# Kernel tuning notes

Measured on AMD Instinct MI355X. Metric: run time of the kernel, lower is better.

## Reference

```python
import jax, jax.numpy as jnp
import numpy as np
import math

D, H, B, T = 1024, 16, 2, 2048
DH = D // H


def setup_inputs() -> dict:
    key = jax.random.key(0)
    ks = jax.random.split(key, 9)
    s = 1.0 / math.sqrt(D)
    x = jax.random.normal(ks[0], (B, T, D), dtype=jnp.float32)
    # True = masked position (masked_fill semantics); causal mask broadcast over b, h
    mask = jnp.triu(jnp.ones((T, T), dtype=bool), k=1)[None, None, :, :]
    wq = jax.random.normal(ks[1], (D, D), dtype=jnp.float32) * s
    bq = jnp.zeros((D,), dtype=jnp.float32)
    wk = jax.random.normal(ks[2], (D, D), dtype=jnp.float32) * s
    bk = jnp.zeros((D,), dtype=jnp.float32)
    wv = jax.random.normal(ks[3], (D, D), dtype=jnp.float32) * s
    bv = jnp.zeros((D,), dtype=jnp.float32)
    wo = jax.random.normal(ks[4], (D, D), dtype=jnp.float32) * s
    bo = jnp.zeros((D,), dtype=jnp.float32)
    return {"x": x, "mask": mask, "wq": wq, "bq": bq, "wk": wk, "bk": bk,
            "wv": wv, "bv": bv, "wo": wo, "bo": bo}


def _rotate_half(u):
    h = u.shape[-1] // 2
    return jnp.concatenate([-u[..., h:], u[..., :h]], axis=-1)


def _sincos(t, dh, dtype):
    pos = jnp.arange(t, dtype=dtype)[:, None]                    # [t, 1]
    inv = 1.0 / (10000.0 ** (jnp.arange(0, dh, 2, dtype=dtype) / dh))  # [dh/2]
    ang = pos * inv                                              # [t, dh/2]
    sin = jnp.repeat(jnp.sin(ang), 2, axis=-1)                   # [t, dh]
    cos = jnp.repeat(jnp.cos(ang), 2, axis=-1)
    return sin, cos


def reference(x, mask, wq, bq, wk, bk, wv, bv, wo, bo):
    b, t, d = x.shape
    h, dh = H, DH
    def heads(u):  # [b,t,d] -> [b,h,t,dh]
        return u.reshape(b, t, h, dh).transpose(0, 2, 1, 3)
    q = heads(x @ wq + bq)
    k = heads(x @ wk + bk)
    v = heads(x @ wv + bv)
    sin, cos = _sincos(t, dh, x.dtype)                           # [t, dh]
    q = q * cos + _rotate_half(q) * sin
    k = k * cos + _rotate_half(k) * sin
    a = jnp.einsum('bhqd,bhkd->bhqk', q, k) / jnp.sqrt(jnp.asarray(dh, x.dtype))
    a = jnp.where(mask, jnp.asarray(-10000.0, x.dtype), a)
    a = jax.nn.softmax(a, axis=-1)                               # dropout p=0.0 -> identity
    out = jnp.einsum('bhqk,bhkd->bhqd', a, v)
    out = out.transpose(0, 2, 1, 3).reshape(b, t, d)
    return out @ wo + bo
```

## Files before the change

### kernel.cpp

```cpp
#include <hip/hip_runtime.h>
#include <hip/hip_bf16.h>

#define DD 1024
#define HH 16
#define BB 2
#define TT 2048
#define DHH 64
#define MM (BB * TT)
#define NQT (TT / 64)
#define BKG 32

typedef __attribute__((ext_vector_type(8))) short bfrag;
typedef __attribute__((ext_vector_type(4))) float ffrag;

__device__ __forceinline__ unsigned short f2bf(float f) {
    __hip_bfloat16 h = __float2bfloat16(f);
    return *reinterpret_cast<unsigned short*>(&h);
}

__device__ __forceinline__ void gl_lds16(const unsigned short* g, unsigned short* l) {
    __builtin_amdgcn_global_load_lds(
        (const __attribute__((address_space(1))) unsigned int*)g,
        (__attribute__((address_space(3))) unsigned int*)l, 16, 0, 0);
}

__global__ __launch_bounds__(256) void prepass_kernel(
    const float* __restrict__ x, unsigned short* __restrict__ xb,
    const float* __restrict__ wq, const float* __restrict__ wk,
    const float* __restrict__ wv, const float* __restrict__ wo,
    unsigned short* __restrict__ oq, unsigned short* __restrict__ ok,
    unsigned short* __restrict__ ov, unsigned short* __restrict__ oo,
    float2* __restrict__ rope_tab)
{
    __shared__ float T[64][65];
    const int z = blockIdx.z;
    const int t = threadIdx.x;
    if (z == 4) {
        const int bid = blockIdx.y * 16 + blockIdx.x;
#pragma unroll
        for (int g = 0; g < 16; ++g) {
            int i = bid * 4096 + g * 256 + t;
            float4 v = ((const float4*)x)[i];
            ushort4 o;
            o.x = f2bf(v.x); o.y = f2bf(v.y); o.z = f2bf(v.z); o.w = f2bf(v.w);
            ((ushort4*)xb)[i] = o;
        }
        int idx = bid * 256 + t;
        int tpos = idx >> 5, i = idx & 31;
        float inv = __expf(-(float)i * (9.210340371976184f / 32.0f));
        float ang = (float)tpos * inv;
        float sv, cv;
        sincosf(ang, &sv, &cv);
        rope_tab[idx] = make_float2(cv, sv);
        return;
    }
    const float* W    = (z == 0) ? wq : (z == 1) ? wk : (z == 2) ? wv : wo;
    unsigned short* O = (z == 0) ? oq : (z == 1) ? ok : (z == 2) ? ov : oo;
    const int n0 = blockIdx.x * 64, k0 = blockIdx.y * 64;
#pragma unroll
    for (int g = 0; g < 16; ++g) {
        int idx = g * 256 + t;
        int r = idx >> 6, c = idx & 63;
        T[c][r] = W[(size_t)(k0 + r) * DD + n0 + c];
    }
    __syncthreads();
#pragma unroll
    for (int g = 0; g < 16; ++g) {
        int idx = g * 256 + t;
        int r = idx >> 6, c = idx & 63;
        O[(size_t)(n0 + r) * DD + k0 + c] = f2bf(T[r][c]);
    }
}

__device__ __forceinline__ void gemm128(
    const unsigned short* __restrict__ X, const unsigned short* __restrict__ Wt,
    int m0, int n0, unsigned short* As, unsigned short* Bs, ffrag acc[4][4])
{
    const int t  = threadIdx.x;
    const int l  = t & 63, w = t >> 6;
    const int lm = l & 15, lq = l >> 4;
    const int wr = w >> 1, wc = w & 1;
    const int srow = l >> 2;
    const int scol = (l & 3) * 8;
#pragma unroll
    for (int m = 0; m < 4; ++m)
#pragma unroll
        for (int n = 0; n < 4; ++n) acc[m][n] = (ffrag){0.f, 0.f, 0.f, 0.f};

    for (int k0 = 0; k0 < DD; k0 += BKG) {
#pragma unroll
        for (int it = 0; it < 2; ++it) {
            const int row = (w * 2 + it) * 16 + srow;
            gl_lds16(&X [(size_t)(m0 + row) * DD + k0 + scol], &As[(w * 2 + it) * 512]);
            gl_lds16(&Wt[(size_t)(n0 + row) * DD + k0 + scol], &Bs[(w * 2 + it) * 512]);
        }
        __syncthreads();
        bfrag a[4], b[4];
#pragma unroll
        for (int m = 0; m < 4; ++m)
            a[m] = *(const bfrag*)&As[(wr * 64 + m * 16 + lm) * BKG + lq * 8];
#pragma unroll
        for (int n = 0; n < 4; ++n)
            b[n] = *(const bfrag*)&Bs[(wc * 64 + n * 16 + lm) * BKG + lq * 8];
#pragma unroll
        for (int m = 0; m < 4; ++m)
#pragma unroll
            for (int n = 0; n < 4; ++n)
                acc[m][n] = __builtin_amdgcn_mfma_f32_16x16x32_bf16(a[m], b[n], acc[m][n], 0, 0, 0);
        __syncthreads();
    }
}

__global__ __launch_bounds__(256) void qkv_rope_kernel(
    const unsigned short* __restrict__ xb,
    const unsigned short* __restrict__ wt_qkv,
    const float* __restrict__ bq, const float* __restrict__ bk,
    const float* __restrict__ bv, const float2* __restrict__ rope_tab,
    unsigned short* __restrict__ Qh, unsigned short* __restrict__ Kh,
    unsigned short* __restrict__ Vh)
{
    __shared__ __align__(16) unsigned short As[128 * BKG];
    __shared__ __align__(16) unsigned short Bs[128 * BKG];
    const int n0 = blockIdx.x * 128, m0 = blockIdx.y * 128;
    ffrag acc[4][4];
    gemm128(xb, wt_qkv, m0, n0, As, Bs, acc);

    const int t  = threadIdx.x;
    const int l  = t & 63, w = t >> 6;
    const int lm = l & 15, lq = l >> 4;
    const int wr = w >> 1, wc = w & 1;
    const int ncol0 = n0 + wc * 64;
    const int which = ncol0 >> 10;
    const float* bias   = (which == 0) ? bq : (which == 1) ? bk : bv;
    unsigned short* Out = (which == 0) ? Qh : (which == 1) ? Kh : Vh;
    const int h = (ncol0 & 1023) >> 6;

    float bv4[4];
#pragma unroll
    for (int n = 0; n < 4; ++n) bv4[n] = bias[(ncol0 & 1023) + n * 16 + lm];

#pragma unroll
    for (int m = 0; m < 4; ++m) {
#pragma unroll
        for (int r = 0; r < 4; ++r) {
            const int row  = m0 + wr * 64 + m * 16 + lq * 4 + r;
            const int b    = row >> 11;
            const int tpos = row & 2047;
            const int bh   = b * HH + h;
#pragma unroll
            for (int n = 0; n < 4; ++n) {
                const int j = n * 16 + lm;
                float val = acc[m][n][r] + bv4[n];
                if (which < 2) {
                    float pair = acc[m][n ^ 2][r] + bv4[n ^ 2];
                    float rh   = (j < 32) ? -pair : pair;
                    float2 cs  = rope_tab[tpos * 32 + (j >> 1)];
                    Out[((size_t)bh * TT + tpos) * DHH + j] = f2bf(val * cs.x + rh * cs.y);
                } else {
                    Out[((size_t)bh * DHH + j) * TT + tpos] = f2bf(val);
                }
            }
        }
    }
}

__global__ __launch_bounds__(256) void attn_kernel(
    const unsigned short* __restrict__ Qh, const unsigned short* __restrict__ Kh,
    const unsigned short* __restrict__ Vh, unsigned short* __restrict__ attn_out)
{
    __shared__ __align__(16) unsigned short Ks[2][64][72];
    __shared__ __align__(16) unsigned short Vt[2][64][72];
    __shared__ __align__(16) unsigned short Pl[4][16][72];

    const int bh = blockIdx.y;
    const int t  = threadIdx.x;
    const int l  = t & 63, w = t >> 6;
    const int lm = l & 15, lq = l >> 4;
    const int r0 = t >> 3, c0 = (t & 7) * 8;
    const float SCALE = 0.125f * 1.4426950408889634f;

    const unsigned short* Qb = Qh + (size_t)bh * TT * DHH;
    const unsigned short* Kb = Kh + (size_t)bh * TT * DHH;
    const unsigned short* Vb = Vh + (size_t)bh * DHH * TT;

    const bfrag onesf = (bfrag){0x3F80, 0x3F80, 0x3F80, 0x3F80,
                                0x3F80, 0x3F80, 0x3F80, 0x3F80};
    const int b = bh >> 4, h = bh & 15;

#pragma unroll 1
    for (int pi = 0; pi < 2; ++pi) {
        const int qt  = (pi == 0) ? (NQT - 1 - blockIdx.x) : blockIdx.x;
        const int q0  = qt * 64, wm0 = q0 + w * 16;

        bfrag qf[2];
#pragma unroll
        for (int kc = 0; kc < 2; ++kc)
            qf[kc] = *(const bfrag*)&Qb[(size_t)(wm0 + lm) * DHH + kc * 32 + lq * 8];

        ffrag o[4];
#pragma unroll
        for (int s = 0; s < 4; ++s) o[s] = (ffrag){0.f, 0.f, 0.f, 0.f};
        ffrag lacc = (ffrag){0.f, 0.f, 0.f, 0.f};

        uint4 pk0, pk1, pv0, pv1;
        pk0 = *(const uint4*)&Kb[(size_t)(r0) * DHH + c0];
        pk1 = *(const uint4*)&Kb[(size_t)(r0 + 32) * DHH + c0];
        pv0 = *(const uint4*)&Vb[(size_t)r0 * TT + c0];
        pv1 = *(const uint4*)&Vb[(size_t)(r0 + 32) * TT + c0];
        *(uint4*)&Ks[0][r0][c0]      = pk0;
        *(uint4*)&Ks[0][r0 + 32][c0] = pk1;
        *(uint4*)&Vt[0][r0][c0]      = pv0;
        *(uint4*)&Vt[0][r0 + 32][c0] = pv1;
        __syncthreads();

        const int nkt = qt + 1;
        for (int kt = 0; kt < nkt; ++kt) {
            const int cur = kt & 1;
            const bool pf = (kt + 1 < nkt);
            if (pf) {
                const int k1 = (kt + 1) * 64;
                pk0 = *(const uint4*)&Kb[(size_t)(k1 + r0) * DHH + c0];
                pk1 = *(const uint4*)&Kb[(size_t)(k1 + r0 + 32) * DHH + c0];
                pv0 = *(const uint4*)&Vb[(size_t)r0 * TT + k1 + c0];
                pv1 = *(const uint4*)&Vb[(size_t)(r0 + 32) * TT + k1 + c0];
            }
            const int k0 = kt * 64;

            float sv[4][4];
#pragma unroll
            for (int s = 0; s < 4; ++s) {
                ffrag sa = (ffrag){0.f, 0.f, 0.f, 0.f};
#pragma unroll
                for (int kc = 0; kc < 2; ++kc) {
                    bfrag bb = *(const bfrag*)&Ks[cur][s * 16 + lm][kc * 32 + lq * 8];
                    sa = __builtin_amdgcn_mfma_f32_16x16x32_bf16(qf[kc], bb, sa, 0, 0, 0);
                }
#pragma unroll
                for (int r = 0; r < 4; ++r)
                    sv[s][r] = sa[r] * SCALE;
            }
            if (kt == qt) {
#pragma unroll
                for (int s = 0; s < 4; ++s) {
                    const int col = k0 + s * 16 + lm;
#pragma unroll
                    for (int r = 0; r < 4; ++r) {
                        const int rowg = wm0 + lq * 4 + r;
                        if (col > rowg) sv[s][r] = -1e30f;
                    }
                }
            }
#pragma unroll
            for (int s = 0; s < 4; ++s)
#pragma unroll
                for (int r = 0; r < 4; ++r)
                    sv[s][r] = exp2f(sv[s][r]);
#pragma unroll
            for (int s = 0; s < 4; ++s) {
                const int ssw = (s ^ ((4 - lq) & 3)) * 16 + lm;
#pragma unroll
                for (int r = 0; r < 4; ++r)
                    Pl[w][lq * 4 + r][ssw] = f2bf(sv[s][r]);
            }
            asm volatile("s_waitcnt lgkmcnt(0)" ::: "memory");
            const int gsw = (4 - (lm >> 2)) & 3;
#pragma unroll
            for (int kc = 0; kc < 2; ++kc) {
                const int scol = ((kc * 2 + (lq >> 1)) ^ gsw) * 16 + (lq & 1) * 8;
                bfrag a = *(const bfrag*)&Pl[w][lm][scol];
#pragma unroll
                for (int s = 0; s < 4; ++s) {
                    bfrag bb = *(const bfrag*)&Vt[cur][s * 16 + lm][kc * 32 + lq * 8];
                    o[s] = __builtin_amdgcn_mfma_f32_16x16x32_bf16(a, bb, o[s], 0, 0, 0);
                }
                lacc = __builtin_amdgcn_mfma_f32_16x16x32_bf16(a, onesf, lacc, 0, 0, 0);
            }
            if (pf) {
                *(uint4*)&Ks[cur ^ 1][r0][c0]      = pk0;
                *(uint4*)&Ks[cur ^ 1][r0 + 32][c0] = pk1;
                *(uint4*)&Vt[cur ^ 1][r0][c0]      = pv0;
                *(uint4*)&Vt[cur ^ 1][r0 + 32][c0] = pv1;
            }
            __syncthreads();
        }

#pragma unroll
        for (int r = 0; r < 4; ++r) {
            const int trow = wm0 + lq * 4 + r;
            const float linv = 1.0f / lacc[r];
#pragma unroll
            for (int s = 0; s < 4; ++s) {
                float ov = o[s][r] * linv;
                attn_out[(((size_t)b * TT + trow) * HH + h) * DHH + s * 16 + lm] = f2bf(ov);
            }
        }
    }
}

__global__ __launch_bounds__(256) void oproj_kernel(
    const unsigned short* __restrict__ attn, const unsigned short* __restrict__ wto,
    const float* __restrict__ bo, float* __restrict__ out)
{
    __shared__ __align__(16) unsigned short As[128 * BKG];
    __shared__ __align__(16) unsigned short Bs[128 * BKG];
    const int n0 = blockIdx.x * 128, m0 = blockIdx.y * 128;
    ffrag acc[4][4];
    gemm128(attn, wto, m0, n0, As, Bs, acc);

    const int t  = threadIdx.x;
    const int l  = t & 63, w = t >> 6;
    const int lm = l & 15, lq = l >> 4;
    const int wr = w >> 1, wc = w & 1;
#pragma unroll
    for (int n = 0; n < 4; ++n) {
        const int col = n0 + wc * 64 + n * 16 + lm;
        const float bb = bo[col];
#pragma unroll
        for (int m = 0; m < 4; ++m)
#pragma unroll
            for (int r = 0; r < 4; ++r) {
                const int row = m0 + wr * 64 + m * 16 + lq * 4 + r;
                out[(size_t)row * DD + col] = acc[m][n][r] + bb;
            }
    }
}

extern "C" void kernel_launch(void* const* d_in, const int* in_sizes, int n_in,
                              void* d_out, int out_size, void* d_ws, size_t ws_size,
                              hipStream_t stream) {
    const float* x  = (const float*)d_in[0];
    const float* wq = (const float*)d_in[2];
    const float* bq = (const float*)d_in[3];
    const float* wk = (const float*)d_in[4];
    const float* bk = (const float*)d_in[5];
    const float* wv = (const float*)d_in[6];
    const float* bv = (const float*)d_in[7];
    const float* wo = (const float*)d_in[8];
    const float* bo = (const float*)d_in[9];

    const size_t perT = (size_t)BB * HH * TT * DHH;
    const size_t perW = (size_t)DD * DD;
    unsigned short* xb   = (unsigned short*)d_ws;
    unsigned short* wtq  = xb  + perT;
    unsigned short* wtk  = wtq + perW;
    unsigned short* wtv  = wtk + perW;
    unsigned short* wto  = wtv + perW;
    unsigned short* Qh   = wto + perW;
    unsigned short* Kh   = Qh + perT;
    unsigned short* Vh   = Kh + perT;
    unsigned short* attn = Vh + perT;
    float2* rope_tab     = (float2*)(attn + perT);

    prepass_kernel<<<dim3(16, 16, 5), 256, 0, stream>>>(
        x, xb, wq, wk, wv, wo, wtq, wtk, wtv, wto, rope_tab);
    qkv_rope_kernel<<<dim3(24, 32), 256, 0, stream>>>(
        xb, wtq, bq, bk, bv, rope_tab, Qh, Kh, Vh);
    attn_kernel<<<dim3(NQT / 2, 32), 256, 0, stream>>>(Qh, Kh, Vh, attn);
    oproj_kernel<<<dim3(8, 32), 256, 0, stream>>>(attn, wto, bo, (float*)d_out);
}
```

Before: 227.2 us.

## Software-pipeline PV matmul one tile behind QK with double-buffered P

```diff
diff --git a/kernel.cpp b/kernel.cpp
--- a/kernel.cpp
+++ b/kernel.cpp
@@ -170,7 +170,7 @@
 {
     __shared__ __align__(16) unsigned short Ks[2][64][72];
     __shared__ __align__(16) unsigned short Vt[2][64][72];
-    __shared__ __align__(16) unsigned short Pl[4][16][72];
+    __shared__ __align__(16) unsigned short Pl[2][4][16][72];
 
     const int bh = blockIdx.y;
     const int t  = threadIdx.x;
@@ -186,6 +186,7 @@
     const bfrag onesf = (bfrag){0x3F80, 0x3F80, 0x3F80, 0x3F80,
                                 0x3F80, 0x3F80, 0x3F80, 0x3F80};
     const int b = bh >> 4, h = bh & 15;
+    const int gsw = (4 - (lm >> 2)) & 3;
 
 #pragma unroll 1
     for (int pi = 0; pi < 2; ++pi) {
@@ -202,29 +203,27 @@
         for (int s = 0; s < 4; ++s) o[s] = (ffrag){0.f, 0.f, 0.f, 0.f};
         ffrag lacc = (ffrag){0.f, 0.f, 0.f, 0.f};
 
-        uint4 pk0, pk1, pv0, pv1;
-        pk0 = *(const uint4*)&Kb[(size_t)(r0) * DHH + c0];
-        pk1 = *(const uint4*)&Kb[(size_t)(r0 + 32) * DHH + c0];
-        pv0 = *(const uint4*)&Vb[(size_t)r0 * TT + c0];
-        pv1 = *(const uint4*)&Vb[(size_t)(r0 + 32) * TT + c0];
-        *(uint4*)&Ks[0][r0][c0]      = pk0;
-        *(uint4*)&Ks[0][r0 + 32][c0] = pk1;
-        *(uint4*)&Vt[0][r0][c0]      = pv0;
-        *(uint4*)&Vt[0][r0 + 32][c0] = pv1;
+        {
+            uint4 a0 = *(const uint4*)&Kb[(size_t)(r0) * DHH + c0];
+            uint4 a1 = *(const uint4*)&Kb[(size_t)(r0 + 32) * DHH + c0];
+            *(uint4*)&Ks[0][r0][c0]      = a0;
+            *(uint4*)&Ks[0][r0 + 32][c0] = a1;
+        }
         __syncthreads();
 
         const int nkt = qt + 1;
+#pragma unroll 1
         for (int kt = 0; kt < nkt; ++kt) {
             const int cur = kt & 1;
-            const bool pf = (kt + 1 < nkt);
-            if (pf) {
-                const int k1 = (kt + 1) * 64;
-                pk0 = *(const uint4*)&Kb[(size_t)(k1 + r0) * DHH + c0];
-                pk1 = *(const uint4*)&Kb[(size_t)(k1 + r0 + 32) * DHH + c0];
-                pv0 = *(const uint4*)&Vb[(size_t)r0 * TT + k1 + c0];
-                pv1 = *(const uint4*)&Vb[(size_t)(r0 + 32) * TT + k1 + c0];
-            }
-            const int k0 = kt * 64;
+            const int k0  = kt * 64;
+            uint4 nk0, nk1, nv0, nv1;
+            const bool pfk = (kt < qt);
+            if (pfk) {
+                nk0 = *(const uint4*)&Kb[(size_t)(k0 + 64 + r0) * DHH + c0];
+                nk1 = *(const uint4*)&Kb[(size_t)(k0 + 64 + r0 + 32) * DHH + c0];
+            }
+            nv0 = *(const uint4*)&Vb[(size_t)r0 * TT + k0 + c0];
+            nv1 = *(const uint4*)&Vb[(size_t)(r0 + 32) * TT + k0 + c0];
 
             float sv[4][4];
 #pragma unroll
@@ -255,34 +254,54 @@
 #pragma unroll
                 for (int r = 0; r < 4; ++r)
                     sv[s][r] = exp2f(sv[s][r]);
+
+            if (kt > 0) {
+                const int prv = cur ^ 1;
+#pragma unroll
+                for (int kc = 0; kc < 2; ++kc) {
+                    const int scol = ((kc * 2 + (lq >> 1)) ^ gsw) * 16 + (lq & 1) * 8;
+                    bfrag a = *(const bfrag*)&Pl[prv][w][lm][scol];
+#pragma unroll
+                    for (int s = 0; s < 4; ++s) {
+                        bfrag bb = *(const bfrag*)&Vt[prv][s * 16 + lm][kc * 32 + lq * 8];
+                        o[s] = __builtin_amdgcn_mfma_f32_16x16x32_bf16(a, bb, o[s], 0, 0, 0);
+                    }
+                    lacc = __builtin_amdgcn_mfma_f32_16x16x32_bf16(a, onesf, lacc, 0, 0, 0);
+                }
+            }
+
 #pragma unroll
             for (int s = 0; s < 4; ++s) {
                 const int ssw = (s ^ ((4 - lq) & 3)) * 16 + lm;
 #pragma unroll
                 for (int r = 0; r < 4; ++r)
-                    Pl[w][lq * 4 + r][ssw] = f2bf(sv[s][r]);
-            }
-            asm volatile("s_waitcnt lgkmcnt(0)" ::: "memory");
-            const int gsw = (4 - (lm >> 2)) & 3;
+                    Pl[cur][w][lq * 4 + r][ssw] = f2bf(sv[s][r]);
+            }
+
+            if (pfk) {
+                *(uint4*)&Ks[cur ^ 1][r0][c0]      = nk0;
+                *(uint4*)&Ks[cur ^ 1][r0 + 32][c0] = nk1;
+            }
+            *(uint4*)&Vt[cur][r0][c0]      = nv0;
+            *(uint4*)&Vt[cur][r0 + 32][c0] = nv1;
+            __syncthreads();
+        }
+
+        {
+            const int prv = qt & 1;
 #pragma unroll
             for (int kc = 0; kc < 2; ++kc) {
                 const int scol = ((kc * 2 + (lq >> 1)) ^ gsw) * 16 + (lq & 1) * 8;
-                bfrag a = *(const bfrag*)&Pl[w][lm][scol];
+                bfrag a = *(const bfrag*)&Pl[prv][w][lm][scol];
 #pragma unroll
                 for (int s = 0; s < 4; ++s) {
-                    bfrag bb = *(const bfrag*)&Vt[cur][s * 16 + lm][kc * 32 + lq * 8];
+                    bfrag bb = *(const bfrag*)&Vt[prv][s * 16 + lm][kc * 32 + lq * 8];
                     o[s] = __builtin_amdgcn_mfma_f32_16x16x32_bf16(a, bb, o[s], 0, 0, 0);
                 }
                 lacc = __builtin_amdgcn_mfma_f32_16x16x32_bf16(a, onesf, lacc, 0, 0, 0);
             }
-            if (pf) {
-                *(uint4*)&Ks[cur ^ 1][r0][c0]      = pk0;
-                *(uint4*)&Ks[cur ^ 1][r0 + 32][c0] = pk1;
-                *(uint4*)&Vt[cur ^ 1][r0][c0]      = pv0;
-                *(uint4*)&Vt[cur ^ 1][r0 + 32][c0] = pv1;
-            }
-            __syncthreads();
-        }
+        }
+        __syncthreads();
 
 #pragma unroll
         for (int r = 0; r < 4; ++r) {
```

New measurement: 227.7 us. No clear change (+0.2%).

## Keep P in registers via shuffles, fold softmax scale into Q RoPE

Applied to the files above, without the earlier changes.

```diff
diff --git a/kernel.cpp b/kernel.cpp
--- a/kernel.cpp
+++ b/kernel.cpp
@@ -30,7 +30,7 @@
     const float* __restrict__ wv, const float* __restrict__ wo,
     unsigned short* __restrict__ oq, unsigned short* __restrict__ ok,
     unsigned short* __restrict__ ov, unsigned short* __restrict__ oo,
-    float2* __restrict__ rope_tab)
+    float4* __restrict__ rope_tab)
 {
     __shared__ float T[64][65];
     const int z = blockIdx.z;
@@ -51,7 +51,8 @@
         float ang = (float)tpos * inv;
         float sv, cv;
         sincosf(ang, &sv, &cv);
-        rope_tab[idx] = make_float2(cv, sv);
+        const float S = 0.125f * 1.4426950408889634f;
+        rope_tab[idx] = make_float4(cv, sv, S * cv, S * sv);
         return;
     }
     const float* W    = (z == 0) ? wq : (z == 1) ? wk : (z == 2) ? wv : wo;
@@ -115,7 +116,7 @@
     const unsigned short* __restrict__ xb,
     const unsigned short* __restrict__ wt_qkv,
     const float* __restrict__ bq, const float* __restrict__ bk,
-    const float* __restrict__ bv, const float2* __restrict__ rope_tab,
+    const float* __restrict__ bv, const float4* __restrict__ rope_tab,
     unsigned short* __restrict__ Qh, unsigned short* __restrict__ Kh,
     unsigned short* __restrict__ Vh)
 {
@@ -151,14 +152,17 @@
             for (int n = 0; n < 4; ++n) {
                 const int j = n * 16 + lm;
                 float val = acc[m][n][r] + bv4[n];
+                float outv;
                 if (which < 2) {
                     float pair = acc[m][n ^ 2][r] + bv4[n ^ 2];
                     float rh   = (j < 32) ? -pair : pair;
-                    float2 cs  = rope_tab[tpos * 32 + (j >> 1)];
-                    Out[((size_t)bh * TT + tpos) * DHH + j] = f2bf(val * cs.x + rh * cs.y);
+                    float4 cs  = rope_tab[tpos * 32 + (j >> 1)];
+                    outv = (which == 0) ? (val * cs.z + rh * cs.w)
+                                        : (val * cs.x + rh * cs.y);
                 } else {
-                    Out[((size_t)bh * DHH + j) * TT + tpos] = f2bf(val);
-                }
+                    outv = val;
+                }
+                Out[((size_t)bh * TT + tpos) * DHH + j] = f2bf(outv);
             }
         }
     }
@@ -170,27 +174,30 @@
 {
     __shared__ __align__(16) unsigned short Ks[2][64][72];
     __shared__ __align__(16) unsigned short Vt[2][64][72];
-    __shared__ __align__(16) unsigned short Pl[4][16][72];
 
     const int bh = blockIdx.y;
     const int t  = threadIdx.x;
     const int l  = t & 63, w = t >> 6;
     const int lm = l & 15, lq = l >> 4;
-    const int r0 = t >> 3, c0 = (t & 7) * 8;
-    const float SCALE = 0.125f * 1.4426950408889634f;
+    const int g  = t >> 3;
+    const int c0 = (t & 7) * 8;
 
     const unsigned short* Qb = Qh + (size_t)bh * TT * DHH;
     const unsigned short* Kb = Kh + (size_t)bh * TT * DHH;
-    const unsigned short* Vb = Vh + (size_t)bh * DHH * TT;
+    const unsigned short* Vb = Vh + (size_t)bh * TT * DHH;
 
     const bfrag onesf = (bfrag){0x3F80, 0x3F80, 0x3F80, 0x3F80,
                                 0x3F80, 0x3F80, 0x3F80, 0x3F80};
     const int b = bh >> 4, h = bh & 15;
+    const int srcA = (2 * (lq & 1)) * 16 + lm;
+    const int srcB = srcA + 16;
+    const bool sig = (lq >> 1) != 0;
 
 #pragma unroll 1
     for (int pi = 0; pi < 2; ++pi) {
-        const int qt  = (pi == 0) ? (NQT - 1 - blockIdx.x) : blockIdx.x;
+        const int qt  = (pi == 0) ? (NQT - 1 - (int)blockIdx.x) : (int)blockIdx.x;
         const int q0  = qt * 64, wm0 = q0 + w * 16;
+        const int rowg = wm0 + lm;
 
         bfrag qf[2];
 #pragma unroll
@@ -202,27 +209,37 @@
         for (int s = 0; s < 4; ++s) o[s] = (ffrag){0.f, 0.f, 0.f, 0.f};
         ffrag lacc = (ffrag){0.f, 0.f, 0.f, 0.f};
 
-        uint4 pk0, pk1, pv0, pv1;
-        pk0 = *(const uint4*)&Kb[(size_t)(r0) * DHH + c0];
-        pk1 = *(const uint4*)&Kb[(size_t)(r0 + 32) * DHH + c0];
-        pv0 = *(const uint4*)&Vb[(size_t)r0 * TT + c0];
-        pv1 = *(const uint4*)&Vb[(size_t)(r0 + 32) * TT + c0];
-        *(uint4*)&Ks[0][r0][c0]      = pk0;
-        *(uint4*)&Ks[0][r0 + 32][c0] = pk1;
-        *(uint4*)&Vt[0][r0][c0]      = pv0;
-        *(uint4*)&Vt[0][r0 + 32][c0] = pv1;
+        {
+            uint4 ka  = *(const uint4*)&Kb[(size_t)(g) * DHH + c0];
+            uint4 kb2 = *(const uint4*)&Kb[(size_t)(g + 32) * DHH + c0];
+            uint4 va  = *(const uint4*)&Vb[(size_t)(2 * g) * DHH + c0];
+            uint4 vb2 = *(const uint4*)&Vb[(size_t)(2 * g + 1) * DHH + c0];
+            *(uint4*)&Ks[0][g][c0]      = ka;
+            *(uint4*)&Ks[0][g + 32][c0] = kb2;
+            const unsigned short* as = (const unsigned short*)&va;
+            const unsigned short* bs = (const unsigned short*)&vb2;
+#pragma unroll
+            for (int j = 0; j < 8; ++j) {
+                unsigned int wp = (unsigned int)as[j] | ((unsigned int)bs[j] << 16);
+                const int dh = c0 + j;
+                const int ch = (g >> 2) ^ ((dh >> 3) & 7);
+                *(unsigned int*)&Vt[0][dh][ch * 8 + (g & 3) * 2] = wp;
+            }
+        }
         __syncthreads();
 
         const int nkt = qt + 1;
+#pragma unroll 1
         for (int kt = 0; kt < nkt; ++kt) {
             const int cur = kt & 1;
-            const bool pf = (kt + 1 < nkt);
+            const bool pf = (kt < qt);
+            uint4 ka, kb2, va, vb2;
             if (pf) {
                 const int k1 = (kt + 1) * 64;
-                pk0 = *(const uint4*)&Kb[(size_t)(k1 + r0) * DHH + c0];
-                pk1 = *(const uint4*)&Kb[(size_t)(k1 + r0 + 32) * DHH + c0];
-                pv0 = *(const uint4*)&Vb[(size_t)r0 * TT + k1 + c0];
-                pv1 = *(const uint4*)&Vb[(size_t)(r0 + 32) * TT + k1 + c0];
+                ka  = *(const uint4*)&Kb[(size_t)(k1 + g) * DHH + c0];
+                kb2 = *(const uint4*)&Kb[(size_t)(k1 + g + 32) * DHH + c0];
+                va  = *(const uint4*)&Vb[(size_t)(k1 + 2 * g) * DHH + c0];
+                vb2 = *(const uint4*)&Vb[(size_t)(k1 + 2 * g + 1) * DHH + c0];
             }
             const int k0 = kt * 64;
 
@@ -232,54 +249,72 @@
                 ffrag sa = (ffrag){0.f, 0.f, 0.f, 0.f};
 #pragma unroll
                 for (int kc = 0; kc < 2; ++kc) {
-                    bfrag bb = *(const bfrag*)&Ks[cur][s * 16 + lm][kc * 32 + lq * 8];
-                    sa = __builtin_amdgcn_mfma_f32_16x16x32_bf16(qf[kc], bb, sa, 0, 0, 0);
-                }
-#pragma unroll
-                for (int r = 0; r < 4; ++r)
-                    sv[s][r] = sa[r] * SCALE;
+                    bfrag kf = *(const bfrag*)&Ks[cur][s * 16 + lm][kc * 32 + lq * 8];
+                    sa = __builtin_amdgcn_mfma_f32_16x16x32_bf16(kf, qf[kc], sa, 0, 0, 0);
+                }
+#pragma unroll
+                for (int r = 0; r < 4; ++r) sv[s][r] = sa[r];
             }
             if (kt == qt) {
 #pragma unroll
-                for (int s = 0; s < 4; ++s) {
-                    const int col = k0 + s * 16 + lm;
+                for (int s = 0; s < 4; ++s)
 #pragma unroll
                     for (int r = 0; r < 4; ++r) {
-                        const int rowg = wm0 + lq * 4 + r;
+                        const int col = k0 + s * 16 + lq * 4 + r;
                         if (col > rowg) sv[s][r] = -1e30f;
                     }
-                }
             }
 #pragma unroll
             for (int s = 0; s < 4; ++s)
 #pragma unroll
                 for (int r = 0; r < 4; ++r)
-                    sv[s][r] = exp2f(sv[s][r]);
-#pragma unroll
-            for (int s = 0; s < 4; ++s) {
-                const int ssw = (s ^ ((4 - lq) & 3)) * 16 + lm;
-#pragma unroll
-                for (int r = 0; r < 4; ++r)
-                    Pl[w][lq * 4 + r][ssw] = f2bf(sv[s][r]);
-            }
-            asm volatile("s_waitcnt lgkmcnt(0)" ::: "memory");
-            const int gsw = (4 - (lm >> 2)) & 3;
+                    sv[s][r] = __builtin_amdgcn_exp2f(sv[s][r]);
+
+            unsigned int pk[8];
+#pragma unroll
+            for (int s = 0; s < 4; ++s)
+#pragma unroll
+                for (int p = 0; p < 2; ++p)
+                    asm("v_cvt_pk_bf16_f32 %0, %1, %2"
+                        : "=v"(pk[s * 2 + p])
+                        : "v"(sv[s][2 * p]), "v"(sv[s][2 * p + 1]));
+
+            uint4 paw[2];
+#pragma unroll
+            for (int kc = 0; kc < 2; ++kc)
+#pragma unroll
+                for (int m = 0; m < 4; ++m) {
+                    const int src = (m & 2) ? srcB : srcA;
+                    unsigned int w0 = (unsigned int)__shfl((int)pk[kc * 4 + (m & 1)], src, 64);
+                    unsigned int w1 = (unsigned int)__shfl((int)pk[kc * 4 + 2 + (m & 1)], src, 64);
+                    ((unsigned int*)&paw[kc])[m] = sig ? w1 : w0;
+                }
+
 #pragma unroll
             for (int kc = 0; kc < 2; ++kc) {
-                const int scol = ((kc * 2 + (lq >> 1)) ^ gsw) * 16 + (lq & 1) * 8;
-                bfrag a = *(const bfrag*)&Pl[w][lm][scol];
+                bfrag pa = *(const bfrag*)&paw[kc];
 #pragma unroll
                 for (int s = 0; s < 4; ++s) {
-                    bfrag bb = *(const bfrag*)&Vt[cur][s * 16 + lm][kc * 32 + lq * 8];
-                    o[s] = __builtin_amdgcn_mfma_f32_16x16x32_bf16(a, bb, o[s], 0, 0, 0);
-                }
-                lacc = __builtin_amdgcn_mfma_f32_16x16x32_bf16(a, onesf, lacc, 0, 0, 0);
-            }
+                    const int ch = (kc * 4 + lq) ^ ((s * 2 + (lm >> 3)) & 7);
+                    bfrag vf = *(const bfrag*)&Vt[cur][s * 16 + lm][ch * 8];
+                    o[s] = __builtin_amdgcn_mfma_f32_16x16x32_bf16(pa, vf, o[s], 0, 0, 0);
+                }
+                lacc = __builtin_amdgcn_mfma_f32_16x16x32_bf16(pa, onesf, lacc, 0, 0, 0);
+            }
+
             if (pf) {
-                *(uint4*)&Ks[cur ^ 1][r0][c0]      = pk0;
-                *(uint4*)&Ks[cur ^ 1][r0 + 32][c0] = pk1;
-                *(uint4*)&Vt[cur ^ 1][r0][c0]      = pv0;
-                *(uint4*)&Vt[cur ^ 1][r0 + 32][c0] = pv1;
+                const int nxt = cur ^ 1;
+                *(uint4*)&Ks[nxt][g][c0]      = ka;
+                *(uint4*)&Ks[nxt][g + 32][c0] = kb2;
+                const unsigned short* as = (const unsigned short*)&va;
+                const unsigned short* bs = (const unsigned short*)&vb2;
+#pragma unroll
+                for (int j = 0; j < 8; ++j) {
+                    unsigned int wp = (unsigned int)as[j] | ((unsigned int)bs[j] << 16);
+                    const int dh = c0 + j;
+                    const int ch = (g >> 2) ^ ((dh >> 3) & 7);
+                    *(unsigned int*)&Vt[nxt][dh][ch * 8 + (g & 3) * 2] = wp;
+                }
             }
             __syncthreads();
         }
@@ -294,6 +329,7 @@
                 attn_out[(((size_t)b * TT + trow) * HH + h) * DHH + s * 16 + lm] = f2bf(ov);
             }
         }
+        __syncthreads();
     }
 }
 
@@ -349,7 +385,7 @@
     unsigned short* Kh   = Qh + perT;
     unsigned short* Vh   = Kh + perT;
     unsigned short* attn = Vh + perT;
-    float2* rope_tab     = (float2*)(attn + perT);
+    float4* rope_tab     = (float4*)(attn + perT);
 
     prepass_kernel<<<dim3(16, 16, 5), 256, 0, stream>>>(
         x, xb, wq, wk, wv, wo, wtq, wtk, wtv, wto, rope_tab);
```

Result: faster. 221.9 us (-2.3%).
